# Kernel tuning notes

Hardware: AMD Instinct MI355X
Metric: run time of the kernel (lower is better)

Reference implementation:

```python
import jax, jax.numpy as jnp
import numpy as np

B, N, C, K = 8, 2048, 64, 32
RADIUS = 0.2
DENSITY_K = 16
INTRINSIC_DIM = 3
NORMALIZE_DP = True
EPS = 1e-8
BN_EPS = 1e-5


def _cdist(x, y):
    # safe euclidean cdist: (..., I, C), (..., J, C) -> (..., I, J)
    d2 = (jnp.sum(x * x, -1)[..., :, None] + jnp.sum(y * y, -1)[..., None, :]
          - 2.0 * jnp.einsum('...ic,...jc->...ij', x, y))
    d2 = jnp.maximum(d2, 0.0)
    safe = jnp.where(d2 > 0, d2, 1.0)
    return jnp.where(d2 > 0, jnp.sqrt(safe), 0.0)


def _ball_query(coords):
    dists = _cdist(coords, coords)                      # (B,N,N)
    _, knn_idx = jax.lax.top_k(-dists, K)               # k smallest
    masked = jnp.where(dists > RADIUS, jnp.inf, dists)
    neg_vals, m_idx = jax.lax.top_k(-masked, K)
    valid = jnp.isfinite(-neg_vals)
    return jnp.where(valid, m_idx, knn_idx)             # (B,N,K)


def _density_weights(grouped):
    # grouped: (B,M,K,3)
    gd = _cdist(grouped, grouped)                       # (B,M,K,K)
    eye = jnp.eye(K, dtype=bool)
    gd = jnp.where(eye, jnp.inf, gd)
    kth = -jax.lax.top_k(-gd, DENSITY_K)[0][..., -1]    # (B,M,K) k-th NN dist
    raw = jnp.maximum(kth, EPS) ** INTRINSIC_DIM
    return raw / jnp.maximum(jnp.sum(raw, -1, keepdims=True), EPS)


def setup_inputs() -> dict:
    key = jax.random.key(0)
    k1, k2, k3 = jax.random.split(key, 3)
    return {
        'coords': jax.random.uniform(k1, (B, N, 3), dtype=jnp.float32),
        'feats': jax.random.normal(k2, (B, C, N), dtype=jnp.float32),
        'conv_w': jax.random.normal(k3, (C, C + 3), dtype=jnp.float32) * 0.05,
        'bn_gamma': jnp.ones((C,), jnp.float32),
        'bn_beta': jnp.zeros((C,), jnp.float32),
        'bn_mean': jnp.zeros((C,), jnp.float32),
        'bn_var': jnp.ones((C,), jnp.float32),
    }


def reference(coords, feats, conv_w, bn_gamma, bn_beta, bn_mean, bn_var):
    idx = _ball_query(coords)                                   # (B,N,K)
    grouped_coords = jax.vmap(lambda c, i: c[i])(coords, idx)   # (B,N,K,3)
    rel = grouped_coords - coords[:, :, None, :]
    if NORMALIZE_DP and RADIUS > 0:
        rel = rel / RADIUS
    grouped_feats = jax.vmap(lambda f, i: f[:, i])(feats, idx)  # (B,C,N,K)
    x = jnp.concatenate([jnp.transpose(rel, (0, 3, 1, 2)), grouped_feats], axis=1)  # (B,C+3,N,K)
    y = jnp.einsum('oc,bcmk->bomk', conv_w, x)                  # 1x1 conv, no bias
    inv = bn_gamma / jnp.sqrt(bn_var + BN_EPS)
    y = y * inv[None, :, None, None] + (bn_beta - bn_mean * inv)[None, :, None, None]
    y = jax.nn.relu(y)
    w = _density_weights(grouped_coords)                        # (B,N,K)
    return jnp.sum(y * w[:, None, :, :], axis=-1)               # (B,C,N)
```

## Files before the change

kernel.cpp:

```cpp
#include <hip/hip_runtime.h>
#include <stdint.h>

#define BB 8
#define NN 2048
#define CC 64
#define KK 32
#define DK 16
#define RADIUSF 0.2f
#define EPSF 1e-8f
#define BN_EPSF 1e-5f

typedef unsigned long long u64;
typedef unsigned int u32;

__device__ __forceinline__ float refsq3(float a, float b, float c) {
  return __fadd_rn(__fadd_rn(__fmul_rn(a, a), __fmul_rn(b, b)), __fmul_rn(c, c));
}
__device__ __forceinline__ float refdot3(float ax, float ay, float az,
                                         float bx, float by, float bz) {
  return __builtin_fmaf(az, bz, __builtin_fmaf(ay, by, __fmul_rn(ax, bx)));
}
__device__ __forceinline__ float refdist(float sx, float sy, float dt) {
  float d2 = __fsub_rn(__fadd_rn(sx, sy), __fmul_rn(2.0f, dt));
  d2 = fmaxf(d2, 0.0f);
  return d2 > 0.0f ? __fsqrt_rn(d2) : 0.0f;
}

#define WAVE_SORT64(V)                                                        \
  {                                                                           \
    _Pragma("unroll") for (int k_ = 2; k_ <= 64; k_ <<= 1) {                  \
      _Pragma("unroll") for (int j_ = k_ >> 1; j_ >= 1; j_ >>= 1) {           \
        __typeof__(V) o_ = __shfl_xor(V, j_);                                 \
        bool keepmin_ = ((lane & k_) == 0) == ((lane & j_) == 0);             \
        __typeof__(V) mn_ = V < o_ ? V : o_;                                  \
        __typeof__(V) mx_ = V < o_ ? o_ : V;                                  \
        V = keepmin_ ? mn_ : mx_;                                             \
      }                                                                       \
    }                                                                         \
  }

__global__ __launch_bounds__(256) void pack_kernel(const float* __restrict__ coords,
                                                   float4* __restrict__ P) {
  int t = blockIdx.x * 256 + threadIdx.x;
  float x = coords[t * 3 + 0], y = coords[t * 3 + 1], z = coords[t * 3 + 2];
  P[t] = make_float4(x, y, z, refsq3(x, y, z));
}

__global__ __launch_bounds__(256) void gfeat_kernel(
    const float* __restrict__ feats, const float* __restrict__ conv_w,
    const float* __restrict__ gamma, const float* __restrict__ beta,
    const float* __restrict__ mean, const float* __restrict__ var,
    float* __restrict__ G) {
  __shared__ float wlds[64 * 65];
  for (int e = threadIdx.x; e < 4096; e += 256) {
    int c = e >> 6, cp = e & 63;
    wlds[c * 65 + cp] = conv_w[c * (CC + 3) + 3 + cp];
  }
  __syncthreads();
  int t = blockIdx.x * 256 + threadIdx.x;
  int c = t & 63;
  int m = t >> 6;
  int b = m >> 11;
  int n = m & (NN - 1);
  float inv = __fdiv_rn(gamma[c], __fsqrt_rn(__fadd_rn(var[c], BN_EPSF)));
  float shift = __fsub_rn(beta[c], __fmul_rn(mean[c], inv));
  const float* f = feats + (size_t)b * CC * NN + n;
  float acc = 0.f;
#pragma unroll
  for (int cp = 0; cp < CC; ++cp) acc = fmaf(wlds[c * 65 + cp], f[(size_t)cp * NN], acc);
  G[t] = fmaf(inv, acc, shift);
}

__global__ __launch_bounds__(256) void knn_kernel(const float4* __restrict__ P,
                                                  int* __restrict__ idx_out) {
  __shared__ u64 surv[4 * 64];
  const int lane = threadIdx.x & 63;
  const int wv = threadIdx.x >> 6;
  const int pid = blockIdx.x * 4 + wv;
  const int b = pid >> 11;
  const int i = pid & (NN - 1);
  const float4* Pb = P + ((size_t)b << 11);
  float4 q = Pb[i];
  u64* sv = surv + wv * 64;
  const u64 lml = (1ull << lane) - 1ull;

  u32 du2[32];
  u32 m0 = 0xFFFFFFFFu;
#pragma unroll
  for (int c = 0; c < 32; ++c) {
    int j = (c << 6) | lane;
    float4 p = Pb[j];
    float dt = refdot3(q.x, q.y, q.z, p.x, p.y, p.z);
    float d2 = __fsub_rn(__fadd_rn(q.w, p.w), __fmul_rn(2.0f, dt));
    d2 = fmaxf(d2, 0.0f);
    u32 s = __float_as_uint(d2);
    du2[c] = s;
    m0 = s < m0 ? s : m0;
  }

  u32 Av = m0;
  WAVE_SORT64(Av);
  const u32 T2 = __shfl(Av, 31) + 4u;

  u32 cls = 0;
#pragma unroll
  for (int c = 0; c < 32; ++c) cls += (du2[c] <= T2) ? 1u : 0u;
  u32 v2 = cls;
#pragma unroll
  for (int sft = 1; sft < 64; sft <<= 1) {
    u32 o = __shfl_up(v2, sft, 64);
    if (lane >= sft) v2 += o;
  }
  const u32 ntot = __shfl(v2, 63);
  int* op = idx_out + (size_t)pid * KK;

  if (ntot <= 64) {
    u32 pos = v2 - cls;
#pragma unroll
    for (int c = 0; c < 32; ++c) {
      if (du2[c] <= T2) {
        sv[pos] = ((u64)du2[c] << 32) | (u64)(u32)((c << 6) | lane);
        ++pos;
      }
    }
    u64 x = ~0ull;
    if (lane < (int)ntot) {
      u64 raw = sv[lane];
      float d2f = __uint_as_float((u32)(raw >> 32));
      u32 dbits = d2f > 0.f ? __float_as_uint(__fsqrt_rn(d2f)) : 0u;
      x = ((u64)dbits << 32) | (raw & 0xFFFFFFFFull);
    }
    WAVE_SORT64(x);
    if (lane < KK) op[lane] = (int)((u32)x & 0x7FFu);
  } else {
#pragma unroll
    for (int c = 0; c < 32; ++c) {
      float d2f = __uint_as_float(du2[c]);
      du2[c] = d2f > 0.f ? __float_as_uint(__fsqrt_rn(d2f)) : 0u;
    }
    u32 ans = 0;
#pragma unroll 1
    for (int bbit = 30; bbit >= 0; --bbit) {
      u32 t2 = ans | (1u << bbit);
      u32 c2 = 0;
#pragma unroll
      for (int c = 0; c < 32; ++c) c2 += (du2[c] < t2) ? 1u : 0u;
#pragma unroll
      for (int sft = 1; sft < 64; sft <<= 1) c2 += __shfl_xor(c2, sft);
      if (c2 < KK) ans = t2;
    }
    const u32 D = ans;
    u32 cntL = 0;
#pragma unroll
    for (int c = 0; c < 32; ++c) cntL += (du2[c] < D) ? 1u : 0u;
    u32 vL = cntL;
#pragma unroll
    for (int sft = 1; sft < 64; sft <<= 1) {
      u32 o = __shfl_up(vL, sft, 64);
      if (lane >= sft) vL += o;
    }
    const u32 r = KK - __shfl(vL, 63);
    u32 pos = vL - cntL;
#pragma unroll
    for (int c = 0; c < 32; ++c) {
      if (du2[c] < D) { op[pos] = (c << 6) | lane; ++pos; }
    }
    u32 emit = r;
    u32 wpos = KK - r;
#pragma unroll
    for (int c = 0; c < 32; ++c) {
      if (emit != 0) {
        u64 mk = __ballot(du2[c] == D);
        u32 pc = (u32)__popcll(mk);
        u32 rk = (u32)__popcll(mk & lml);
        if ((du2[c] == D) && rk < emit) op[wpos + rk] = (c << 6) | lane;
        u32 take = pc < emit ? pc : emit;
        wpos += take;
        emit -= take;
      }
    }
  }
}

__global__ __launch_bounds__(256) void dagg_kernel(
    const float4* __restrict__ P, const float* __restrict__ conv_w,
    const float* __restrict__ gamma, const float* __restrict__ var,
    const float* __restrict__ G, const int* __restrict__ idxb,
    float* __restrict__ out) {
  __shared__ float4 ldsRW[4][64];
  __shared__ int ldsJ[4][64];
  const int lane = threadIdx.x & 63;
  const int wv = threadIdx.x >> 6;
  const int half = lane >> 5;
  const int k = lane & 31;
  const int pid_pair = blockIdx.x * 8 + wv * 2;
  const int pid = pid_pair + half;
  const int b = pid >> 11;
  const float4* Pb = P + ((size_t)b << 11);

  const int i = pid & (NN - 1);
  float4 q = Pb[i];
  int jk = idxb[(size_t)pid * KK + k];
  float4 nb = Pb[jk];

  float rx = __fdiv_rn(__fsub_rn(nb.x, q.x), RADIUSF);
  float ry = __fdiv_rn(__fsub_rn(nb.y, q.y), RADIUSF);
  float rz = __fdiv_rn(__fsub_rn(nb.z, q.z), RADIUSF);

  u32 d2b[32];
#pragma unroll
  for (int t = 0; t < 32; ++t) {
    float ox = __shfl(nb.x, t, 32);
    float oy = __shfl(nb.y, t, 32);
    float oz = __shfl(nb.z, t, 32);
    float so = __shfl(nb.w, t, 32);
    float dt = refdot3(nb.x, nb.y, nb.z, ox, oy, oz);
    float d2 = __fsub_rn(__fadd_rn(nb.w, so), __fmul_rn(2.0f, dt));
    d2 = fmaxf(d2, 0.0f);
    d2b[t] = (t == k) ? 0x7F800000u : __float_as_uint(d2);
  }
#pragma unroll
  for (int p = 1; p < 32; p <<= 1) {
#pragma unroll
    for (int kk = p; kk >= 1; kk >>= 1) {
#pragma unroll
      for (int jj = (kk & (p - 1)); jj + kk < 32; jj += 2 * kk) {
#pragma unroll
        for (int t = 0; t < kk; ++t) {
          if ((t + jj) / (2 * p) == (t + jj + kk) / (2 * p)) {
            u32 a = d2b[t + jj], b2 = d2b[t + jj + kk];
            d2b[t + jj] = a < b2 ? a : b2;
            d2b[t + jj + kk] = a < b2 ? b2 : a;
          }
        }
      }
    }
  }
  float kd2 = __uint_as_float(d2b[DK - 1]);
  float kth = kd2 > 0.f ? __fsqrt_rn(kd2) : 0.f;
  float r1 = fmaxf(kth, EPSF);
  float raw = __fmul_rn(__fmul_rn(r1, r1), r1);
  float s = raw;
#pragma unroll
  for (int t = 1; t < 32; t <<= 1) s += __shfl_xor(s, t, 32);
  float wk = raw / fmaxf(s, EPSF);

  ldsRW[wv][lane] = make_float4(rx, ry, rz, wk);
  ldsJ[wv][lane] = jk * 64;

  float inv = __fdiv_rn(gamma[lane], __fsqrt_rn(__fadd_rn(var[lane], BN_EPSF)));
  float w0 = conv_w[lane * (CC + 3) + 0] * inv;
  float w1 = conv_w[lane * (CC + 3) + 1] * inv;
  float w2 = conv_w[lane * (CC + 3) + 2] * inv;
  const float* Gb = G + ((size_t)b * NN) * 64 + lane;

#pragma unroll
  for (int h2 = 0; h2 < 2; ++h2) {
    const int pid2 = pid_pair + h2;
    const int i2 = pid2 & (NN - 1);
    float acc = 0.f;
#pragma unroll
    for (int kk2 = 0; kk2 < KK; ++kk2) {
      float4 rw = ldsRW[wv][h2 * 32 + kk2];
      int joff = ldsJ[wv][h2 * 32 + kk2];
      float g = Gb[joff];
      float y = fmaf(w2, rw.z, fmaf(w1, rw.y, fmaf(w0, rw.x, g)));
      y = fmaxf(y, 0.f);
      acc = fmaf(rw.w, y, acc);
    }
    out[((size_t)(b * 64 + lane)) * NN + i2] = acc;
  }
}

extern "C" void kernel_launch(void* const* d_in, const int* in_sizes, int n_in,
                              void* d_out, int out_size, void* d_ws, size_t ws_size,
                              hipStream_t stream) {
  const float* coords = (const float*)d_in[0];
  const float* feats  = (const float*)d_in[1];
  const float* conv_w = (const float*)d_in[2];
  const float* gamma  = (const float*)d_in[3];
  const float* beta   = (const float*)d_in[4];
  const float* mean   = (const float*)d_in[5];
  const float* var    = (const float*)d_in[6];
  float* out = (float*)d_out;

  int*   idxb = (int*)d_ws;
  float4* P   = (float4*)((char*)d_ws + (size_t)2 * 1024 * 1024);
  float* G    = (float*)((char*)d_ws + (size_t)4 * 1024 * 1024);

  const int NPTS = BB * NN;

  pack_kernel<<<NPTS / 256, 256, 0, stream>>>(coords, P);
  knn_kernel<<<NPTS / 4, 256, 0, stream>>>(P, idxb);
  gfeat_kernel<<<(NPTS * CC) / 256, 256, 0, stream>>>(feats, conv_w, gamma, beta,
                                                      mean, var, G);
  dagg_kernel<<<NPTS / 8, 256, 0, stream>>>(P, conv_w, gamma, var, G, idxb, out);
}
```

Measured before the change: 80.61 us.

## Replace wave bitonic sorts and shuffle scans with LDS rank counting

Replaces the in-wave bitonic sort used for the threshold selection and the final 64-element sort with rank-by-counting over values staged in shared memory, read back as vector loads. The shuffle-based prefix scan is likewise replaced by each lane summing the shared counts. The aim is to cut the long dependent chains of cross-lane shuffles in exchange for more LDS reads and compares per lane. Correctness relies on wave-synchronous execution with only __threadfence_block between the LDS write and read phases.

```diff
diff --git a/kernel.cpp b/kernel.cpp
--- a/kernel.cpp
+++ b/kernel.cpp
@@ -25,19 +25,6 @@
   d2 = fmaxf(d2, 0.0f);
   return d2 > 0.0f ? __fsqrt_rn(d2) : 0.0f;
 }
-
-#define WAVE_SORT64(V)                                                        \
-  {                                                                           \
-    _Pragma("unroll") for (int k_ = 2; k_ <= 64; k_ <<= 1) {                  \
-      _Pragma("unroll") for (int j_ = k_ >> 1; j_ >= 1; j_ >>= 1) {           \
-        __typeof__(V) o_ = __shfl_xor(V, j_);                                 \
-        bool keepmin_ = ((lane & k_) == 0) == ((lane & j_) == 0);             \
-        __typeof__(V) mn_ = V < o_ ? V : o_;                                  \
-        __typeof__(V) mx_ = V < o_ ? o_ : V;                                  \
-        V = keepmin_ ? mn_ : mx_;                                             \
-      }                                                                       \
-    }                                                                         \
-  }
 
 __global__ __launch_bounds__(256) void pack_kernel(const float* __restrict__ coords,
                                                    float4* __restrict__ P) {
@@ -73,7 +60,9 @@
 
 __global__ __launch_bounds__(256) void knn_kernel(const float4* __restrict__ P,
                                                   int* __restrict__ idx_out) {
-  __shared__ u64 surv[4 * 64];
+  __shared__ __align__(16) u64 sv[4][64];
+  __shared__ __align__(16) u32 aux[4][64];
+  __shared__ u32 tslv[4];
   const int lane = threadIdx.x & 63;
   const int wv = threadIdx.x >> 6;
   const int pid = blockIdx.x * 4 + wv;
@@ -81,7 +70,6 @@
   const int i = pid & (NN - 1);
   const float4* Pb = P + ((size_t)b << 11);
   float4 q = Pb[i];
-  u64* sv = surv + wv * 64;
   const u64 lml = (1ull << lane) - 1ull;
 
   u32 du2[32];
@@ -98,40 +86,71 @@
     m0 = s < m0 ? s : m0;
   }
 
-  u32 Av = m0;
-  WAVE_SORT64(Av);
-  const u32 T2 = __shfl(Av, 31) + 4u;
+  aux[wv][lane] = m0;
+  __threadfence_block();
+  const uint4* a4 = (const uint4*)(&aux[wv][0]);
+  u32 rkm = 0;
+#pragma unroll
+  for (int t4 = 0; t4 < 16; ++t4) {
+    uint4 v = a4[t4];
+    int e = t4 << 2;
+    rkm += (v.x < m0 || (v.x == m0 && (e + 0) < lane)) ? 1u : 0u;
+    rkm += (v.y < m0 || (v.y == m0 && (e + 1) < lane)) ? 1u : 0u;
+    rkm += (v.z < m0 || (v.z == m0 && (e + 2) < lane)) ? 1u : 0u;
+    rkm += (v.w < m0 || (v.w == m0 && (e + 3) < lane)) ? 1u : 0u;
+  }
+  if (rkm == 31) tslv[wv] = m0;
+  __threadfence_block();
+  const u32 T2 = tslv[wv] + 4u;
 
   u32 cls = 0;
 #pragma unroll
   for (int c = 0; c < 32; ++c) cls += (du2[c] <= T2) ? 1u : 0u;
-  u32 v2 = cls;
-#pragma unroll
-  for (int sft = 1; sft < 64; sft <<= 1) {
-    u32 o = __shfl_up(v2, sft, 64);
-    if (lane >= sft) v2 += o;
-  }
-  const u32 ntot = __shfl(v2, 63);
+  aux[wv][lane] = cls;
+  __threadfence_block();
+  u32 pre = 0, ntot = 0;
+#pragma unroll
+  for (int t4 = 0; t4 < 16; ++t4) {
+    uint4 v = a4[t4];
+    int e = t4 << 2;
+    ntot += v.x + v.y + v.z + v.w;
+    pre += ((e + 0) < lane) ? v.x : 0u;
+    pre += ((e + 1) < lane) ? v.y : 0u;
+    pre += ((e + 2) < lane) ? v.z : 0u;
+    pre += ((e + 3) < lane) ? v.w : 0u;
+  }
+
   int* op = idx_out + (size_t)pid * KK;
 
   if (ntot <= 64) {
-    u32 pos = v2 - cls;
+    sv[wv][lane] = ~0ull;
+    __threadfence_block();
+    u32 pos = pre;
 #pragma unroll
     for (int c = 0; c < 32; ++c) {
       if (du2[c] <= T2) {
-        sv[pos] = ((u64)du2[c] << 32) | (u64)(u32)((c << 6) | lane);
+        sv[wv][pos & 63] = ((u64)du2[c] << 32) | (u64)(u32)((c << 6) | lane);
         ++pos;
       }
     }
-    u64 x = ~0ull;
+    __threadfence_block();
     if (lane < (int)ntot) {
-      u64 raw = sv[lane];
+      u64 raw = sv[wv][lane];
       float d2f = __uint_as_float((u32)(raw >> 32));
-      u32 dbits = d2f > 0.f ? __float_as_uint(__fsqrt_rn(d2f)) : 0u;
-      x = ((u64)dbits << 32) | (raw & 0xFFFFFFFFull);
-    }
-    WAVE_SORT64(x);
-    if (lane < KK) op[lane] = (int)((u32)x & 0x7FFu);
+      u32 db = d2f > 0.f ? __float_as_uint(__fsqrt_rn(d2f)) : 0u;
+      sv[wv][lane] = ((u64)db << 32) | (raw & 0xFFFFFFFFull);
+    }
+    __threadfence_block();
+    u64 x = sv[wv][lane];
+    const ulonglong2* s2 = (const ulonglong2*)(&sv[wv][0]);
+    u32 rnk = 0;
+#pragma unroll
+    for (int t2 = 0; t2 < 32; ++t2) {
+      ulonglong2 v = s2[t2];
+      rnk += (v.x < x) ? 1u : 0u;
+      rnk += (v.y < x) ? 1u : 0u;
+    }
+    if (lane < (int)ntot && rnk < KK) op[rnk] = (int)((u32)x & 0x7FFu);
   } else {
 #pragma unroll
     for (int c = 0; c < 32; ++c) {
```

New measurement: 88.23 us. 1.09x slower.
